# Kernel optimization log

Hardware: AMD Instinct MI355X
Metric: run time of the kernel (lower is better)

## Reference

```python
import jax, jax.numpy as jnp
import numpy as np

NH = 16
HD = 128
ROPE_THETA = 10000.0


def _rope_tables(L, dtype):
    inv_freq = 1.0 / (ROPE_THETA ** (jnp.arange(0, HD, 2, dtype=jnp.float32) / HD))
    t = jnp.arange(L, dtype=jnp.float32)
    freqs = jnp.outer(t, inv_freq)          # [L, HD/2]
    emb = jnp.concatenate([freqs, freqs], axis=-1)  # [L, HD]
    return jnp.cos(emb).astype(dtype), jnp.sin(emb).astype(dtype)


def _rotate_half(x):
    x1, x2 = jnp.split(x, 2, axis=-1)
    return jnp.concatenate([-x2, x1], axis=-1)


def _apply_rope(x, cos, sin):
    return x * cos + _rotate_half(x) * sin


def setup_inputs() -> dict:
    key = jax.random.key(0)
    k1, k2, k3 = jax.random.split(key, 3)
    B, L, H = 2, 2048, 2048
    x = jax.random.normal(k1, (B, L, H), dtype=jnp.float32)
    w_qkv = jax.random.normal(k2, (3 * H, H), dtype=jnp.float32) * 0.02
    w_o = jax.random.normal(k3, (H, H), dtype=jnp.float32) * 0.02
    return {"x": x, "w_qkv": w_qkv, "w_o": w_o}


def reference(x, w_qkv, w_o):
    B, L, H = x.shape
    qkv = x @ w_qkv.T                                   # [B, L, 3H]
    qkv = qkv.reshape(B, L, 3, NH, HD).transpose(2, 0, 3, 1, 4)  # [3, B, NH, L, HD]
    q, k, v = qkv[0], qkv[1], qkv[2]
    cos, sin = _rope_tables(L, x.dtype)
    cos, sin = cos[None, None], sin[None, None]         # [1, 1, L, HD]
    q = _apply_rope(q, cos, sin)
    k = _apply_rope(k, cos, sin)
    scale = 1.0 / jnp.sqrt(jnp.asarray(HD, dtype=x.dtype))
    scores = jnp.einsum('bhqd,bhkd->bhqk', q, k) * scale
    causal = jnp.tril(jnp.ones((L, L), dtype=bool))
    scores = jnp.where(causal[None, None], scores, jnp.asarray(-1e30, dtype=x.dtype))
    attn = jax.nn.softmax(scores, axis=-1)
    out = jnp.einsum('bhqk,bhkd->bhqd', attn, v)        # [B, NH, L, HD]
    out = out.transpose(0, 2, 1, 3).reshape(B, L, H)
    return out @ w_o.T
```

## Files before the change

kernel.cpp:

```cpp
#include <hip/hip_runtime.h>

#define NHEADS 16
#define HD 128
#define LSEQ 2048
#define NBATCH 2
#define HDIM 2048
#define NQKV 6144
#define SCALE 0.08838834764831845f

typedef __attribute__((ext_vector_type(8))) short bfx8;
typedef __attribute__((ext_vector_type(4))) short bfx4;
typedef __attribute__((ext_vector_type(4))) float f32x4;

__device__ __forceinline__ unsigned short f2bf(float x) {
  unsigned u = __float_as_uint(x);
  u += 0x7fffu + ((u >> 16) & 1u);
  return (unsigned short)(u >> 16);
}
__device__ __forceinline__ float bf2f(unsigned short u) {
  return __uint_as_float(((unsigned)u) << 16);
}
__device__ __forceinline__ void gload_lds16(const void* g, void* l) {
  __builtin_amdgcn_global_load_lds(
      (const __attribute__((address_space(1))) unsigned int*)g,
      (__attribute__((address_space(3))) unsigned int*)l, 16, 0, 0);
}

__global__ __launch_bounds__(256) void cast_bf16_kernel(
    const float* __restrict__ in, unsigned short* __restrict__ out, int n4) {
  int i = blockIdx.x * 256 + threadIdx.x;
  if (i >= n4) return;
  float4 v = ((const float4*)in)[i];
  bfx4 o;
  o[0] = (short)f2bf(v.x);
  o[1] = (short)f2bf(v.y);
  o[2] = (short)f2bf(v.z);
  o[3] = (short)f2bf(v.w);
  ((bfx4*)out)[i] = o;
}

template<bool BF16OUT>
__global__ __launch_bounds__(512, 1) void gemm256_kernel(
    const unsigned short* __restrict__ A, const unsigned short* __restrict__ B,
    void* __restrict__ Cout, int M, int N, int K) {
  __shared__ unsigned short lA[2][256 * 64];
  __shared__ unsigned short lB[2][256 * 64];
  const int tid = threadIdx.x;
  const int w = tid >> 6, lane = tid & 63;
  const int g = lane >> 4, ln = lane & 15;
  const int nmt = M >> 8, nnt = N >> 8;
  const int nwg = nmt * nnt;
  const int bid = blockIdx.x;
  const int swz = (bid & 7) * (nwg >> 3) + (bid >> 3);
  const int bm = (swz / nnt) * 256, bn = (swz % nnt) * 256;
  const int wm = (w >> 2) * 128, wn = (w & 3) * 64;
  const unsigned short* At = A + (size_t)bm * K;
  const unsigned short* Bt = B + (size_t)bn * K;

  auto STG = [&](const unsigned short* src, unsigned short* dst, int q, int k0) {
    int rid = q * 64 + w * 8 + (lane >> 3);
    int slot = lane & 7;
    gload_lds16(src + (size_t)rid * K + k0 + ((slot ^ (rid & 7)) << 3),
                dst + (size_t)(q * 4096 + w * 512));
  };

  f32x4 acc[8][4];
#pragma unroll
  for (int i = 0; i < 8; ++i)
#pragma unroll
    for (int j = 0; j < 4; ++j) acc[i][j] = (f32x4){0.f, 0.f, 0.f, 0.f};

  STG(Bt, lB[0], 0, 0); STG(Bt, lB[0], 1, 0);
  STG(Bt, lB[0], 2, 0); STG(Bt, lB[0], 3, 0);
  STG(At, lA[0], 0, 0); STG(At, lA[0], 2, 0);
  STG(At, lA[0], 1, 0); STG(At, lA[0], 3, 0);
  asm volatile("s_waitcnt vmcnt(2)" ::: "memory");
  __builtin_amdgcn_s_barrier();

  const int nt = K >> 6;
  bfx8 bfrag[4][2];
  for (int t = 0; t < nt; ++t) {
    const int cur = t & 1;
    const char* lAc = (const char*)lA[cur];
    const char* lBc = (const char*)lB[cur];
    unsigned short* sA = lA[cur ^ 1];
    unsigned short* sB = lB[cur ^ 1];
    const int k1 = (t + 1) << 6;
    const bool more = (t + 1 < nt);
#pragma unroll
    for (int ph = 0; ph < 4; ++ph) {
      if (more) {
        if (ph == 0)      { STG(Bt, sB, 0, k1); STG(Bt, sB, 1, k1); }
        else if (ph == 1) { STG(Bt, sB, 2, k1); STG(Bt, sB, 3, k1); }
        else if (ph == 2) { STG(At, sA, 0, k1); STG(At, sA, 2, k1); }
        else              { STG(At, sA, 1, k1); STG(At, sA, 3, k1); }
      }
      bfx8 afrag[2][2];
#pragma unroll
      for (int mi = 0; mi < 2; ++mi)
#pragma unroll
        for (int kk = 0; kk < 2; ++kk)
          afrag[mi][kk] = *(const bfx8*)(lAc + (wm + (ph * 2 + mi) * 16 + ln) * 128 +
                                         (((kk * 4 + g) ^ (ln & 7)) << 4));
      if (ph == 0) {
#pragma unroll
        for (int nf = 0; nf < 4; ++nf)
#pragma unroll
          for (int kk = 0; kk < 2; ++kk)
            bfrag[nf][kk] = *(const bfx8*)(lBc + (wn + nf * 16 + ln) * 128 +
                                           (((kk * 4 + g) ^ (ln & 7)) << 4));
      }
      __builtin_amdgcn_s_barrier();
      asm volatile("s_waitcnt lgkmcnt(0)" ::: "memory");
      __builtin_amdgcn_sched_barrier(0);
      __builtin_amdgcn_s_setprio(1);
#pragma unroll
      for (int kk = 0; kk < 2; ++kk)
#pragma unroll
        for (int mi = 0; mi < 2; ++mi)
#pragma unroll
          for (int nf = 0; nf < 4; ++nf)
            acc[ph * 2 + mi][nf] = __builtin_amdgcn_mfma_f32_16x16x32_bf16(
                afrag[mi][kk], bfrag[nf][kk], acc[ph * 2 + mi][nf], 0, 0, 0);
      __builtin_amdgcn_s_setprio(0);
      if (ph == 1) {
        if (more) asm volatile("s_waitcnt vmcnt(4)" ::: "memory");
        else      asm volatile("s_waitcnt vmcnt(0)" ::: "memory");
      } else if (ph == 3 && more) {
        asm volatile("s_waitcnt vmcnt(2)" ::: "memory");
      }
      __builtin_amdgcn_sched_barrier(0);
      __builtin_amdgcn_s_barrier();
    }
  }

#pragma unroll
  for (int mf = 0; mf < 8; ++mf) {
    int row0 = bm + wm + mf * 16 + g * 4;
#pragma unroll
    for (int nf = 0; nf < 4; ++nf) {
      int col = bn + wn + nf * 16 + ln;
#pragma unroll
      for (int r = 0; r < 4; ++r) {
        if constexpr (BF16OUT)
          ((unsigned short*)Cout)[(size_t)(row0 + r) * N + col] = f2bf(acc[mf][nf][r]);
        else
          ((float*)Cout)[(size_t)(row0 + r) * N + col] = acc[mf][nf][r];
      }
    }
  }
}

template<bool BF16OUT>
__global__ __launch_bounds__(256) void gemm_bt_kernel(
    const unsigned short* __restrict__ A, const unsigned short* __restrict__ B,
    void* __restrict__ Cout, int M, int N, int K) {
  __shared__ unsigned short lA[128 * 64];
  __shared__ unsigned short lB[128 * 64];
  const int tid = threadIdx.x;
  const int w = tid >> 6, lane = tid & 63;
  const int g = lane >> 4, ln = lane & 15;
  const int bm = blockIdx.x * 128, bn = blockIdx.y * 128;
  const int wm = (w >> 1) * 64, wn = (w & 1) * 64;
  const int srow = lane >> 3;
  const int scol = (lane & 7) * 8;

  f32x4 acc[4][4];
#pragma unroll
  for (int i = 0; i < 4; ++i)
#pragma unroll
    for (int j = 0; j < 4; ++j) acc[i][j] = (f32x4){0.f, 0.f, 0.f, 0.f};

  for (int k0 = 0; k0 < K; k0 += 64) {
#pragma unroll
    for (int p = 0; p < 4; ++p) {
      int seg = p * 4 + w;
      int row = seg * 8 + srow;
      const unsigned short* gA = A + (size_t)(bm + row) * K + (k0 + scol);
      const unsigned short* gB = B + (size_t)(bn + row) * K + (k0 + scol);
      gload_lds16(gA, lA + seg * 512);
      gload_lds16(gB, lB + seg * 512);
    }
    __syncthreads();
#pragma unroll
    for (int kk = 0; kk < 2; ++kk) {
      bfx8 af[4], bfr[4];
#pragma unroll
      for (int i = 0; i < 4; ++i)
        af[i] = *(const bfx8*)(lA + (wm + i * 16 + ln) * 64 + kk * 32 + g * 8);
#pragma unroll
      for (int j = 0; j < 4; ++j)
        bfr[j] = *(const bfx8*)(lB + (wn + j * 16 + ln) * 64 + kk * 32 + g * 8);
#pragma unroll
      for (int i = 0; i < 4; ++i)
#pragma unroll
        for (int j = 0; j < 4; ++j)
          acc[i][j] = __builtin_amdgcn_mfma_f32_16x16x32_bf16(af[i], bfr[j], acc[i][j], 0, 0, 0);
    }
    __syncthreads();
  }
#pragma unroll
  for (int i = 0; i < 4; ++i) {
    int row0 = bm + wm + i * 16 + g * 4;
#pragma unroll
    for (int j = 0; j < 4; ++j) {
      int col = bn + wn + j * 16 + ln;
#pragma unroll
      for (int r = 0; r < 4; ++r) {
        if constexpr (BF16OUT)
          ((unsigned short*)Cout)[(size_t)(row0 + r) * N + col] = f2bf(acc[i][j][r]);
        else
          ((float*)Cout)[(size_t)(row0 + r) * N + col] = acc[i][j][r];
      }
    }
  }
}

__global__ __launch_bounds__(256) void rope_scatter_kernel(
    const unsigned short* __restrict__ qkv,
    unsigned short* __restrict__ Qo, unsigned short* __restrict__ Ko,
    unsigned short* __restrict__ Vt) {
  __shared__ unsigned short lV[32 * 128];
  const int bh = blockIdx.x;
  const int l0 = blockIdx.y * 32;
  const int b = bh >> 4, h = bh & 15;
  const int tid = threadIdx.x;
#pragma unroll
  for (int it = 0; it < 2; ++it) {
    int idx = it * 256 + tid;
    int ll = idx >> 4;
    int dq = idx & 15;
    int l = l0 + ll;
    const unsigned short* row = qkv + (size_t)(b * LSEQ + l) * NQKV + h * HD;
    bfx4 qlo = *(const bfx4*)(row + dq * 4);
    bfx4 qhi = *(const bfx4*)(row + 64 + dq * 4);
    bfx4 klo = *(const bfx4*)(row + 2048 + dq * 4);
    bfx4 khi = *(const bfx4*)(row + 2048 + 64 + dq * 4);
    bfx4 vlo = *(const bfx4*)(row + 4096 + dq * 4);
    bfx4 vhi = *(const bfx4*)(row + 4096 + 64 + dq * 4);
    bfx4 oqlo, oqhi, oklo, okhi;
#pragma unroll
    for (int e = 0; e < 4; ++e) {
      int d2 = dq * 4 + e;
      float invf = exp2f(-(float)d2 * 0.2076205059304601f);
      float fr = (float)l * invf;
      float s, c;
      sincosf(fr, &s, &c);
      float xq1 = bf2f((unsigned short)qlo[e]), xq2 = bf2f((unsigned short)qhi[e]);
      oqlo[e] = (short)f2bf(xq1 * c - xq2 * s);
      oqhi[e] = (short)f2bf(xq2 * c + xq1 * s);
      float xk1 = bf2f((unsigned short)klo[e]), xk2 = bf2f((unsigned short)khi[e]);
      oklo[e] = (short)f2bf(xk1 * c - xk2 * s);
      okhi[e] = (short)f2bf(xk2 * c + xk1 * s);
    }
    size_t obase = ((size_t)bh * LSEQ + l) * HD;
    *(bfx4*)(Qo + obase + dq * 4) = oqlo;
    *(bfx4*)(Qo + obase + 64 + dq * 4) = oqhi;
    *(bfx4*)(Ko + obase + dq * 4) = oklo;
    *(bfx4*)(Ko + obase + 64 + dq * 4) = okhi;
    *(bfx4*)(lV + ll * 128 + dq * 4) = vlo;
    *(bfx4*)(lV + ll * 128 + 64 + dq * 4) = vhi;
  }
  __syncthreads();
#pragma unroll
  for (int it = 0; it < 16; ++it) {
    int idx = it * 256 + tid;
    int d = idx >> 5;
    int ll = idx & 31;
    Vt[((size_t)bh * HD + d) * LSEQ + l0 + ll] = lV[ll * 128 + d];
  }
}

__global__ __launch_bounds__(512, 4) void flash_kernel(
    const unsigned short* __restrict__ Q, const unsigned short* __restrict__ K,
    const unsigned short* __restrict__ Vt, unsigned short* __restrict__ O) {
  __shared__ unsigned short lKs[2][64 * 128];
  __shared__ unsigned short lVs[2][128 * 64];
  __shared__ unsigned short lP[8][16 * 40];
  const int bh = blockIdx.x;
  const int qt = 15 - (int)blockIdx.y;
  const int q0 = qt * 128;
  const int tid = threadIdx.x;
  const int w = tid >> 6, lane = tid & 63;
  const int g = lane >> 4, ln = lane & 15;
  const int q0w = q0 + w * 16;
  const unsigned short* Qb = Q + (size_t)bh * LSEQ * HD;
  const unsigned short* Kb = K + (size_t)bh * LSEQ * HD;
  const unsigned short* Vb = Vt + (size_t)bh * HD * LSEQ;
  unsigned short* Pw = lP[w];

  auto STAGE = [&](int buf, int kv0s) {
#pragma unroll
    for (int s = 0; s < 2; ++s) {
      int rl = s * 32 + w * 4 + (lane >> 4);
      int slot = lane & 15;
      const unsigned short* src =
          Kb + (size_t)(kv0s + rl) * HD + ((slot ^ (rl & 15)) * 8);
      gload_lds16(src, &lKs[buf][(s * 8192 + w * 1024) / 2]);
    }
#pragma unroll
    for (int s = 0; s < 2; ++s) {
      int d = s * 64 + w * 8 + (lane >> 3);
      int slot = lane & 7;
      const unsigned short* src =
          Vb + (size_t)d * LSEQ + kv0s + ((slot ^ (d & 7)) * 8);
      gload_lds16(src, &lVs[buf][(s * 8192 + w * 1024) / 2]);
    }
  };

  bfx8 qf[4];
#pragma unroll
  for (int c = 0; c < 4; ++c)
    qf[c] = *(const bfx8*)(Qb + (size_t)(q0w + ln) * HD + c * 32 + g * 8);

  f32x4 o[8];
#pragma unroll
  for (int dt = 0; dt < 8; ++dt) o[dt] = (f32x4){0.f, 0.f, 0.f, 0.f};
  float m = -1e30f, sum = 0.f;
  const int qg = q0w + ln;
  const int nch = 2 * qt + 2;

  STAGE(0, 0);
  __syncthreads();

  for (int ch = 0; ch < nch; ++ch) {
    const int kv0 = ch * 64;
    const int cur = ch & 1;
    if (ch + 1 < nch) STAGE(cur ^ 1, kv0 + 64);

    if (kv0 <= q0w + 15) {
      const char* lK0 = (const char*)lKs[cur];
      const char* lV0 = (const char*)lVs[cur];
      f32x4 s4[4];
#pragma unroll
      for (int kt = 0; kt < 4; ++kt) s4[kt] = (f32x4){0.f, 0.f, 0.f, 0.f};
#pragma unroll
      for (int c = 0; c < 4; ++c) {
        const int cbb = c * 64 + g * 16;
#pragma unroll
        for (int kt = 0; kt < 4; ++kt) {
          bfx8 kf = *(const bfx8*)(lK0 + (kt * 16 + ln) * 256 + (cbb ^ (ln << 4)));
          s4[kt] = __builtin_amdgcn_mfma_f32_16x16x32_bf16(kf, qf[c], s4[kt], 0, 0, 0);
        }
      }
      float tm = -1e30f;
      if (kv0 + 63 <= q0w) {
#pragma unroll
        for (int kt = 0; kt < 4; ++kt)
#pragma unroll
          for (int r = 0; r < 4; ++r) {
            s4[kt][r] *= SCALE;
            tm = fmaxf(tm, s4[kt][r]);
          }
      } else {
#pragma unroll
        for (int kt = 0; kt < 4; ++kt)
#pragma unroll
          for (int r = 0; r < 4; ++r) {
            int kvr = kv0 + kt * 16 + 4 * g + r;
            float v = (kvr <= qg) ? s4[kt][r] * SCALE : -1e30f;
            s4[kt][r] = v;
            tm = fmaxf(tm, v);
          }
      }
      tm = fmaxf(tm, __shfl_xor(tm, 16));
      tm = fmaxf(tm, __shfl_xor(tm, 32));
      float f = 1.f;
      const bool dorescale = !__all(tm <= m + 8.f);
      if (dorescale) {
        float mnew = fmaxf(m, tm);
        f = __expf(m - mnew);
        m = mnew;
      }
      float ts = 0.f;
      bfx4 pb4[4];
#pragma unroll
      for (int kt = 0; kt < 4; ++kt)
#pragma unroll
        for (int r = 0; r < 4; ++r) {
          float p = __expf(s4[kt][r] - m);
          ts += p;
          pb4[kt][r] = (short)f2bf(p);
        }
      ts += __shfl_xor(ts, 16);
      ts += __shfl_xor(ts, 32);
      sum = sum * f + ts;
      float fr0 = 1.f, fr1 = 1.f, fr2 = 1.f, fr3 = 1.f;
      if (dorescale) {
        fr0 = __shfl(f, 4 * g + 0);
        fr1 = __shfl(f, 4 * g + 1);
        fr2 = __shfl(f, 4 * g + 2);
        fr3 = __shfl(f, 4 * g + 3);
      }
#pragma unroll
      for (int kvh = 0; kvh < 2; ++kvh) {
        asm volatile("s_waitcnt lgkmcnt(0)" ::: "memory");
        __builtin_amdgcn_sched_barrier(0);
        *(bfx4*)(Pw + ln * 40 + 4 * g) = pb4[2 * kvh];
        *(bfx4*)(Pw + ln * 40 + 16 + 4 * g) = pb4[2 * kvh + 1];
        asm volatile("s_waitcnt lgkmcnt(0)" ::: "memory");
        __builtin_amdgcn_sched_barrier(0);
        bfx8 pf = *(const bfx8*)(Pw + ln * 40 + g * 8);
        if (kvh == 0 && dorescale) {
#pragma unroll
          for (int dt = 0; dt < 8; ++dt) {
            o[dt][0] *= fr0; o[dt][1] *= fr1; o[dt][2] *= fr2; o[dt][3] *= fr3;
          }
        }
#pragma unroll
        for (int dt = 0; dt < 8; ++dt) {
          bfx8 vf = *(const bfx8*)(lV0 + (dt * 16 + ln) * 128 +
                                   ((kvh * 64 + g * 16) ^ ((ln & 7) << 4)));
          o[dt] = __builtin_amdgcn_mfma_f32_16x16x32_bf16(pf, vf, o[dt], 0, 0, 0);
        }
      }
    }
    __syncthreads();
  }

  float inv = 1.f / sum;
  float ir0 = __shfl(inv, 4 * g + 0);
  float ir1 = __shfl(inv, 4 * g + 1);
  float ir2 = __shfl(inv, 4 * g + 2);
  float ir3 = __shfl(inv, 4 * g + 3);
  const int b = bh >> 4, h = bh & 15;
  unsigned short* Ob = O + (size_t)b * LSEQ * HDIM + h * HD;
#pragma unroll
  for (int dt = 0; dt < 8; ++dt) {
    Ob[(size_t)(q0w + 4 * g + 0) * HDIM + dt * 16 + ln] = f2bf(o[dt][0] * ir0);
    Ob[(size_t)(q0w + 4 * g + 1) * HDIM + dt * 16 + ln] = f2bf(o[dt][1] * ir1);
    Ob[(size_t)(q0w + 4 * g + 2) * HDIM + dt * 16 + ln] = f2bf(o[dt][2] * ir2);
    Ob[(size_t)(q0w + 4 * g + 3) * HDIM + dt * 16 + ln] = f2bf(o[dt][3] * ir3);
  }
}

extern "C" void kernel_launch(void* const* d_in, const int* in_sizes, int n_in,
                              void* d_out, int out_size, void* d_ws, size_t ws_size,
                              hipStream_t stream) {
  const float* x = (const float*)d_in[0];
  const float* w_qkv = (const float*)d_in[1];
  const float* w_o = (const float*)d_in[2];
  float* out = (float*)d_out;
  char* ws = (char*)d_ws;

  unsigned short* xb    = (unsigned short*)(ws + 0);
  unsigned short* wqkvb = (unsigned short*)(ws + 16777216);
  unsigned short* wob   = (unsigned short*)(ws + 41943040);
  unsigned short* qkvb  = (unsigned short*)(ws + 50331648);
  unsigned short* qb    = (unsigned short*)(ws + 100663296);
  unsigned short* kb    = (unsigned short*)(ws + 117440512);
  unsigned short* vtb   = (unsigned short*)(ws + 134217728);
  unsigned short* attnb = (unsigned short*)(ws + 0);

  cast_bf16_kernel<<<8388608 / 4 / 256, 256, 0, stream>>>(x, xb, 8388608 / 4);
  cast_bf16_kernel<<<12582912 / 4 / 256, 256, 0, stream>>>(w_qkv, wqkvb, 12582912 / 4);
  cast_bf16_kernel<<<4194304 / 4 / 256, 256, 0, stream>>>(w_o, wob, 4194304 / 4);

  gemm256_kernel<true><<<(4096 / 256) * (6144 / 256), 512, 0, stream>>>(
      xb, wqkvb, (void*)qkvb, 4096, 6144, 2048);

  rope_scatter_kernel<<<dim3(32, 64), 256, 0, stream>>>(qkvb, qb, kb, vtb);

  flash_kernel<<<dim3(32, 16), 512, 0, stream>>>(qb, kb, vtb, attnb);

  gemm_bt_kernel<false><<<dim3(4096 / 128, 2048 / 128), 256, 0, stream>>>(
      attnb, wob, (void*)out, 4096, 2048, 2048);
}
```

Measured before the change: 301.5 us.

## Parametrize 256-row GEMM N-tile width and use it for QKV and output projections

Templates the pipelined 256xBN GEMM on the N-tile width, using 256x192 tiles for the QKV projection (512 workgroups instead of 384) and 256x128 tiles for the output projection in place of the simple 128x128 kernel. All next-tile loads are now issued at phase 0 with adjusted vmcnt waits, and one barrier per phase is dropped. The aim is better CU fill on the 256-CU device and a faster output GEMM, at the cost of smaller per-block reuse and a changed load/sync schedule that could race if the waits are wrong.

```diff
diff --git a/kernel.cpp b/kernel.cpp
--- a/kernel.cpp
+++ b/kernel.cpp
@@ -39,21 +39,22 @@
   ((bfx4*)out)[i] = o;
 }
 
-template<bool BF16OUT>
+template<int BNQ, bool BF16OUT>
 __global__ __launch_bounds__(512, 1) void gemm256_kernel(
     const unsigned short* __restrict__ A, const unsigned short* __restrict__ B,
     void* __restrict__ Cout, int M, int N, int K) {
+  constexpr int BN = BNQ * 64;
   __shared__ unsigned short lA[2][256 * 64];
-  __shared__ unsigned short lB[2][256 * 64];
+  __shared__ unsigned short lB[2][BN * 64];
   const int tid = threadIdx.x;
   const int w = tid >> 6, lane = tid & 63;
   const int g = lane >> 4, ln = lane & 15;
-  const int nmt = M >> 8, nnt = N >> 8;
+  const int nmt = M >> 8, nnt = N / BN;
   const int nwg = nmt * nnt;
   const int bid = blockIdx.x;
   const int swz = (bid & 7) * (nwg >> 3) + (bid >> 3);
-  const int bm = (swz / nnt) * 256, bn = (swz % nnt) * 256;
-  const int wm = (w >> 2) * 128, wn = (w & 3) * 64;
+  const int bm = (swz / nnt) * 256, bn = (swz % nnt) * BN;
+  const int wm = (w >> 2) * 128, wn = (w & 3) * (BNQ * 16);
   const unsigned short* At = A + (size_t)bm * K;
   const unsigned short* Bt = B + (size_t)bn * K;
 
@@ -63,38 +64,33 @@
     gload_lds16(src + (size_t)rid * K + k0 + ((slot ^ (rid & 7)) << 3),
                 dst + (size_t)(q * 4096 + w * 512));
   };
-
-  f32x4 acc[8][4];
+  auto STAGE_ALL = [&](int buf, int k0) {
+#pragma unroll
+    for (int q = 0; q < BNQ; ++q) STG(Bt, lB[buf], q, k0);
+    STG(At, lA[buf], 0, k0); STG(At, lA[buf], 2, k0);
+    STG(At, lA[buf], 1, k0); STG(At, lA[buf], 3, k0);
+  };
+
+  f32x4 acc[8][BNQ];
 #pragma unroll
   for (int i = 0; i < 8; ++i)
 #pragma unroll
-    for (int j = 0; j < 4; ++j) acc[i][j] = (f32x4){0.f, 0.f, 0.f, 0.f};
-
-  STG(Bt, lB[0], 0, 0); STG(Bt, lB[0], 1, 0);
-  STG(Bt, lB[0], 2, 0); STG(Bt, lB[0], 3, 0);
-  STG(At, lA[0], 0, 0); STG(At, lA[0], 2, 0);
-  STG(At, lA[0], 1, 0); STG(At, lA[0], 3, 0);
+    for (int j = 0; j < BNQ; ++j) acc[i][j] = (f32x4){0.f, 0.f, 0.f, 0.f};
+
+  STAGE_ALL(0, 0);
   asm volatile("s_waitcnt vmcnt(2)" ::: "memory");
   __builtin_amdgcn_s_barrier();
 
   const int nt = K >> 6;
-  bfx8 bfrag[4][2];
+  bfx8 bfrag[BNQ][2];
   for (int t = 0; t < nt; ++t) {
     const int cur = t & 1;
     const char* lAc = (const char*)lA[cur];
     const char* lBc = (const char*)lB[cur];
-    unsigned short* sA = lA[cur ^ 1];
-    unsigned short* sB = lB[cur ^ 1];
-    const int k1 = (t + 1) << 6;
     const bool more = (t + 1 < nt);
 #pragma unroll
     for (int ph = 0; ph < 4; ++ph) {
-      if (more) {
-        if (ph == 0)      { STG(Bt, sB, 0, k1); STG(Bt, sB, 1, k1); }
-        else if (ph == 1) { STG(Bt, sB, 2, k1); STG(Bt, sB, 3, k1); }
-        else if (ph == 2) { STG(At, sA, 0, k1); STG(At, sA, 2, k1); }
-        else              { STG(At, sA, 1, k1); STG(At, sA, 3, k1); }
-      }
+      if (ph == 0 && more) STAGE_ALL(cur ^ 1, (t + 1) << 6);
       bfx8 afrag[2][2];
 #pragma unroll
       for (int mi = 0; mi < 2; ++mi)
@@ -104,13 +100,12 @@
                                          (((kk * 4 + g) ^ (ln & 7)) << 4));
       if (ph == 0) {
 #pragma unroll
-        for (int nf = 0; nf < 4; ++nf)
+        for (int nf = 0; nf < BNQ; ++nf)
 #pragma unroll
           for (int kk = 0; kk < 2; ++kk)
             bfrag[nf][kk] = *(const bfx8*)(lBc + (wn + nf * 16 + ln) * 128 +
                                            (((kk * 4 + g) ^ (ln & 7)) << 4));
       }
-      __builtin_amdgcn_s_barrier();
       asm volatile("s_waitcnt lgkmcnt(0)" ::: "memory");
       __builtin_amdgcn_sched_barrier(0);
       __builtin_amdgcn_s_setprio(1);
@@ -119,13 +114,17 @@
 #pragma unroll
         for (int mi = 0; mi < 2; ++mi)
 #pragma unroll
-          for (int nf = 0; nf < 4; ++nf)
+          for (int nf = 0; nf < BNQ; ++nf)
             acc[ph * 2 + mi][nf] = __builtin_amdgcn_mfma_f32_16x16x32_bf16(
                 afrag[mi][kk], bfrag[nf][kk], acc[ph * 2 + mi][nf], 0, 0, 0);
       __builtin_amdgcn_s_setprio(0);
       if (ph == 1) {
-        if (more) asm volatile("s_waitcnt vmcnt(4)" ::: "memory");
-        else      asm volatile("s_waitcnt vmcnt(0)" ::: "memory");
+        if (more) {
+          if constexpr (BNQ == 3) asm volatile("s_waitcnt vmcnt(7)" ::: "memory");
+          else                    asm volatile("s_waitcnt vmcnt(6)" ::: "memory");
+        } else {
+          asm volatile("s_waitcnt vmcnt(0)" ::: "memory");
+        }
       } else if (ph == 3 && more) {
         asm volatile("s_waitcnt vmcnt(2)" ::: "memory");
       }
@@ -138,7 +137,7 @@
   for (int mf = 0; mf < 8; ++mf) {
     int row0 = bm + wm + mf * 16 + g * 4;
 #pragma unroll
-    for (int nf = 0; nf < 4; ++nf) {
+    for (int nf = 0; nf < BNQ; ++nf) {
       int col = bn + wn + nf * 16 + ln;
 #pragma unroll
       for (int r = 0; r < 4; ++r) {
@@ -146,71 +145,6 @@
           ((unsigned short*)Cout)[(size_t)(row0 + r) * N + col] = f2bf(acc[mf][nf][r]);
         else
           ((float*)Cout)[(size_t)(row0 + r) * N + col] = acc[mf][nf][r];
-      }
-    }
-  }
-}
-
-template<bool BF16OUT>
-__global__ __launch_bounds__(256) void gemm_bt_kernel(
-    const unsigned short* __restrict__ A, const unsigned short* __restrict__ B,
-    void* __restrict__ Cout, int M, int N, int K) {
-  __shared__ unsigned short lA[128 * 64];
-  __shared__ unsigned short lB[128 * 64];
-  const int tid = threadIdx.x;
-  const int w = tid >> 6, lane = tid & 63;
-  const int g = lane >> 4, ln = lane & 15;
-  const int bm = blockIdx.x * 128, bn = blockIdx.y * 128;
-  const int wm = (w >> 1) * 64, wn = (w & 1) * 64;
-  const int srow = lane >> 3;
-  const int scol = (lane & 7) * 8;
-
-  f32x4 acc[4][4];
-#pragma unroll
-  for (int i = 0; i < 4; ++i)
-#pragma unroll
-    for (int j = 0; j < 4; ++j) acc[i][j] = (f32x4){0.f, 0.f, 0.f, 0.f};
-
-  for (int k0 = 0; k0 < K; k0 += 64) {
-#pragma unroll
-    for (int p = 0; p < 4; ++p) {
-      int seg = p * 4 + w;
-      int row = seg * 8 + srow;
-      const unsigned short* gA = A + (size_t)(bm + row) * K + (k0 + scol);
-      const unsigned short* gB = B + (size_t)(bn + row) * K + (k0 + scol);
-      gload_lds16(gA, lA + seg * 512);
-      gload_lds16(gB, lB + seg * 512);
-    }
-    __syncthreads();
-#pragma unroll
-    for (int kk = 0; kk < 2; ++kk) {
-      bfx8 af[4], bfr[4];
-#pragma unroll
-      for (int i = 0; i < 4; ++i)
-        af[i] = *(const bfx8*)(lA + (wm + i * 16 + ln) * 64 + kk * 32 + g * 8);
-#pragma unroll
-      for (int j = 0; j < 4; ++j)
-        bfr[j] = *(const bfx8*)(lB + (wn + j * 16 + ln) * 64 + kk * 32 + g * 8);
-#pragma unroll
-      for (int i = 0; i < 4; ++i)
-#pragma unroll
-        for (int j = 0; j < 4; ++j)
-          acc[i][j] = __builtin_amdgcn_mfma_f32_16x16x32_bf16(af[i], bfr[j], acc[i][j], 0, 0, 0);
-    }
-    __syncthreads();
-  }
-#pragma unroll
-  for (int i = 0; i < 4; ++i) {
-    int row0 = bm + wm + i * 16 + g * 4;
-#pragma unroll
-    for (int j = 0; j < 4; ++j) {
-      int col = bn + wn + j * 16 + ln;
-#pragma unroll
-      for (int r = 0; r < 4; ++r) {
-        if constexpr (BF16OUT)
-          ((unsigned short*)Cout)[(size_t)(row0 + r) * N + col] = f2bf(acc[i][j][r]);
-        else
-          ((float*)Cout)[(size_t)(row0 + r) * N + col] = acc[i][j][r];
       }
     }
   }
@@ -456,13 +390,13 @@
   cast_bf16_kernel<<<12582912 / 4 / 256, 256, 0, stream>>>(w_qkv, wqkvb, 12582912 / 4);
   cast_bf16_kernel<<<4194304 / 4 / 256, 256, 0, stream>>>(w_o, wob, 4194304 / 4);
 
-  gemm256_kernel<true><<<(4096 / 256) * (6144 / 256), 512, 0, stream>>>(
+  gemm256_kernel<3, true><<<(4096 / 256) * (6144 / 192), 512, 0, stream>>>(
       xb, wqkvb, (void*)qkvb, 4096, 6144, 2048);
 
   rope_scatter_kernel<<<dim3(32, 64), 256, 0, stream>>>(qkvb, qb, kb, vtb);
 
   flash_kernel<<<dim3(32, 16), 512, 0, stream>>>(qb, kb, vtb, attnb);
 
-  gemm_bt_kernel<false><<<dim3(4096 / 128, 2048 / 128), 256, 0, stream>>>(
+  gemm256_kernel<2, false><<<(4096 / 256) * (2048 / 128), 512, 0, stream>>>(
       attnb, wob, (void*)out, 4096, 2048, 2048);
 }
```

Measured after the change: 318.5 us. 1.06x slower.
